# Optimization experiments

Measured on AMD Instinct MI355X. Metric: run time of the kernel, lower is better.

The kernel has to match this reference:

```python
import jax, jax.numpy as jnp
import numpy as np

B, S, N, DEG, KC = 4, 12, 8192, 16, 3
SEQ = S - KC + 1  # 10
H, LAYER, HID, MLP_H = 4, 3, 3, 64
NEG = -1e9


def setup_inputs() -> dict:
    key = jax.random.key(0)
    ks = jax.random.split(key, 40)
    f = lambda i, shp, sc=0.2: jax.random.normal(ks[i], shp, jnp.float32) * sc
    # deterministic unique edge list: DEG distinct neighbors per source node
    src = np.repeat(np.arange(N), DEG)
    dst = (src + 1 + np.tile(np.arange(DEG), N) * 37) % N
    edges = jnp.asarray(np.stack([src, dst]).astype(np.int32))
    return dict(
        occ=jax.random.normal(ks[0], (B, S, N), jnp.float32),
        prc_l=jax.random.uniform(ks[1], (B, N), jnp.float32),
        edges=edges,
        values=jnp.ones((N * DEG,), jnp.float32),
        conv_w=f(2, (1, 1, KC, 2)), conv_b=f(3, (1,)),
        gat_W=f(4, (H, SEQ, SEQ)), gat_a=f(5, (H, 2 * SEQ)),
        gat_lin_w=f(6, (1, H)), gat_lin_b=f(7, (1,)),
        gcn_w=f(8, (SEQ, SEQ)), gcn_b=f(9, (SEQ,)),
        Wih0=f(10, (4 * HID, LAYER)), Whh0=f(11, (4 * HID, HID)), bih0=f(12, (4 * HID,)), bhh0=f(13, (4 * HID,)),
        Wih1=f(14, (4 * HID, HID)), Whh1=f(15, (4 * HID, HID)), bih1=f(16, (4 * HID,)), bhh1=f(17, (4 * HID,)),
        Qw=f(18, (SEQ, SEQ)), Kw=f(19, (SEQ, SEQ)), Vw=f(20, (SEQ, SEQ)),
        m1w1=f(21, (MLP_H, SEQ)), m1b1=f(22, (MLP_H,)),
        m1w2=f(23, (MLP_H // 2, MLP_H)), m1b2=f(24, (MLP_H // 2,)),
        m1w3=f(25, (1, MLP_H // 2)), m1b3=f(26, (1,)),
        m2w1=f(27, (8 * (LAYER + 1), LAYER + 1)), m2b1=f(28, (8 * (LAYER + 1),)),
        m2w2=f(29, (4 * (LAYER + 1), 8 * (LAYER + 1))), m2b2=f(30, (4 * (LAYER + 1),)),
        m2w3=f(31, (1, 4 * (LAYER + 1))), m2b3=f(32, (1,)),
    )


def _lstm_layer(x, Wih, Whh, bih, bhh):
    # x: [T, Bn, in] time-major; PyTorch gate order i,f,g,o
    Bn, hdim = x.shape[1], Whh.shape[1]
    def step(carry, xt):
        h, c = carry
        g = xt @ Wih.T + h @ Whh.T + bih + bhh
        i, fg, gg, o = jnp.split(g, 4, axis=1)
        c = jax.nn.sigmoid(fg) * c + jax.nn.sigmoid(i) * jnp.tanh(gg)
        h = jax.nn.sigmoid(o) * jnp.tanh(c)
        return (h, c), h
    init = (jnp.zeros((Bn, hdim), x.dtype), jnp.zeros((Bn, hdim), x.dtype))
    _, hs = jax.lax.scan(step, init, x)
    return hs  # [T, Bn, hdim]


def _gat(x2, src, dst, values, mask, gat_W, gat_a, lin_w, lin_b):
    # x2: [b*n, seq]; only first N rows are gathered (faithful to the original)
    h = jnp.einsum('ns,hso->hno', x2, gat_W)                 # [H, b*n, seq]
    eh = jnp.concatenate([h[:, src, :], h[:, dst, :]], 2)    # [H, E, 2*seq]
    atts = jax.nn.leaky_relu(jnp.einsum('hed,hd->he', eh, gat_a), 0.2)  # [H, E]
    mt = atts.T @ lin_w.T + lin_b                            # [E, 1]
    new_vals = values * mt[:, 0]
    n = mask.shape[0]
    dense = jnp.zeros((n, n), x2.dtype).at[src, dst].add(new_vals)
    return jax.nn.softmax(dense + mask, axis=0)              # softmax over dim 0, as nn.Softmax(dim=0)


def reference(occ, prc_l, edges, values, conv_w, conv_b, gat_W, gat_a, gat_lin_w, gat_lin_b, gcn_w, gcn_b, Wih0, Whh0, bih0, bhh0, Wih1, Whh1, bih1, bhh1, Qw, Kw, Vw, m1w1, m1b1, m1w2, m1b2, m1w3, m1b3, m2w1, m2b1, m2w2, m2b2, m2w3, m2b3):
    b, s, n = occ.shape
    seq = s - conv_w.shape[2] + 1
    occ_t = jnp.transpose(occ, (0, 2, 1))                    # [b, n, s]
    prc = jnp.broadcast_to(prc_l[:, :, None], (b, n, s))
    fea = jnp.stack([occ_t, prc], axis=3).reshape(b * n, s, 2)[:, None]  # [bn,1,s,2]
    fea = jax.lax.conv_general_dilated(fea, conv_w, (1, 1), 'VALID',
                                       dimension_numbers=('NCHW', 'OIHW', 'NCHW'))
    fea = (fea + conv_b[None, :, None, None]).reshape(b, n, seq)
    src, dst = edges[0], edges[1]
    mask = jnp.full((n, n), NEG, occ.dtype).at[src, dst].set(0.0)
    lrelu = lambda z: jax.nn.leaky_relu(z, 0.01)
    gcn = lambda z: lrelu(z @ gcn_w.T + gcn_b)
    A1 = _gat(fea.reshape(b * n, seq), src, dst, values, mask, gat_W, gat_a, gat_lin_w, gat_lin_b)
    c1 = gcn(jnp.einsum('nm,bms->bns', A1, fea))
    A2 = _gat(c1.reshape(b * n, seq), src, dst, values, mask, gat_W, gat_a, gat_lin_w, gat_lin_b)
    c2 = gcn(jnp.einsum('nm,bms->bns', A2, c1))
    xt = jnp.stack([fea, c1, c2], axis=3).reshape(b * n, seq, 3)
    xT = jnp.transpose(xt, (1, 0, 2))                        # time-major [seq, bn, 3]
    h0 = _lstm_layer(xT, Wih0, Whh0, bih0, bhh0)
    h1 = _lstm_layer(h0, Wih1, Whh1, bih1, bhh1)
    x_long = jnp.transpose(h1, (1, 0, 2))                    # [bn, seq, 3]
    y_long = x_long[:, -1, 0]                                # [bn]
    xl = jnp.transpose(x_long, (0, 2, 1))                    # [bn, 3, seq]
    Q = xl @ Qw.T
    K = xl @ Kw.T
    V = xl @ Vw.T
    alpha = jax.nn.softmax(jnp.einsum('bis,bjs->bij', Q, K) / jnp.float32(V.shape[1]), axis=2)
    att = jnp.einsum('bij,bjs->bis', alpha, V)               # [bn, 3, seq]
    h = jax.nn.relu(att @ m1w1.T + m1b1)
    h = jax.nn.relu(h @ m1w2.T + m1b2)
    att_out = (h @ m1w3.T + m1b3)[:, :, 0]                   # [bn, 3]
    temp = jnp.concatenate([y_long[:, None], att_out], axis=1)  # [bn, 4]
    h = jax.nn.relu(temp @ m2w1.T + m2b1)
    h = jax.nn.relu(h @ m2w2.T + m2b2)
    y = (h @ m2w3.T + m2b3)[:, 0]
    return y.reshape(b, n)
```

## Files before the change

### kernel.cpp

```cpp
#include <hip/hip_runtime.h>

#define NN    8192
#define BB    4
#define SS    12
#define SEQL  10
#define SEQP  16
#define KCC   3
#define DEGN  16
#define EE    (NN*DEGN)
#define HHH   4
#define HIDN  3
#define BN    (BB*NN)

__device__ __forceinline__ float fexp(float x)  { return __expf(x); }
__device__ __forceinline__ float fsig(float x)  { return __fdividef(1.0f, 1.0f + __expf(-x)); }

__global__ __launch_bounds__(256) void k_fea_node(const float* __restrict__ occ,
                                                  const float* __restrict__ prc,
                                                  const float* __restrict__ convw,
                                                  const float* __restrict__ convb,
                                                  const float* __restrict__ gatW,
                                                  const float* __restrict__ gata,
                                                  float* __restrict__ fea,
                                                  float* __restrict__ p1p2) {
    int t = blockIdx.x * blockDim.x + threadIdx.x;
    if (t >= BN) return;
    int b = t >> 13, nn = t & (NN - 1);
    float o[SS];
    const float* op = occ + (size_t)b * SS * NN + nn;
#pragma unroll
    for (int s = 0; s < SS; s++) o[s] = op[(size_t)s * NN];
    float w0[KCC], w1s = 0.f;
#pragma unroll
    for (int k = 0; k < KCC; k++) { w0[k] = convw[k * 2]; w1s += convw[k * 2 + 1]; }
    float base = prc[t] * w1s + convb[0];
    float fv[SEQL];
#pragma unroll
    for (int tt = 0; tt < SEQL; tt++) {
        float acc = base;
#pragma unroll
        for (int k = 0; k < KCC; k++) acc += o[tt + k] * w0[k];
        fv[tt] = acc;
    }
    float* f = fea + (size_t)t * SEQP;
    *(float4*)(f)     = make_float4(fv[0], fv[1], fv[2], fv[3]);
    *(float4*)(f + 4) = make_float4(fv[4], fv[5], fv[6], fv[7]);
    *(float2*)(f + 8) = make_float2(fv[8], fv[9]);
    if (t < NN) {
#pragma unroll
        for (int hh = 0; hh < HHH; hh++) {
            float p1 = 0.f, p2 = 0.f;
#pragma unroll
            for (int oo = 0; oo < SEQL; oo++) {
                float hv = 0.f;
#pragma unroll
                for (int s = 0; s < SEQL; s++) hv += fv[s] * gatW[hh * (SEQL * SEQL) + s * SEQL + oo];
                p1 += hv * gata[hh * (2 * SEQL) + oo];
                p2 += hv * gata[hh * (2 * SEQL) + SEQL + oo];
            }
            p1p2[t * 8 + hh]     = p1;
            p1p2[t * 8 + 4 + hh] = p2;
        }
    }
}

__global__ __launch_bounds__(256) void k_colmt(const float* __restrict__ values,
                                               const float* __restrict__ p1p2,
                                               const float* __restrict__ linw,
                                               const float* __restrict__ linb,
                                               float* __restrict__ mt,
                                               float2* __restrict__ colms) {
    int u = blockIdx.x * blockDim.x + threadIdx.x;
    int q = u & 3, j = u >> 2;
    float p2l[HHH], lw[HHH];
#pragma unroll
    for (int hh = 0; hh < HHH; hh++) { p2l[hh] = p1p2[j * 8 + 4 + hh]; lw[hh] = linw[hh]; }
    float lb = linb[0];
    float v[4];
#pragma unroll
    for (int dd = 0; dd < 4; dd++) {
        int d = q * 4 + dd;
        int s = (j - 1 - d * 37) & (NN - 1);
        int e = s * DEGN + d;
        float4 p1v = *(const float4*)(p1p2 + s * 8);
        float a0 = p1v.x + p2l[0]; a0 = a0 > 0.f ? a0 : 0.2f * a0;
        float a1 = p1v.y + p2l[1]; a1 = a1 > 0.f ? a1 : 0.2f * a1;
        float a2 = p1v.z + p2l[2]; a2 = a2 > 0.f ? a2 : 0.2f * a2;
        float a3 = p1v.w + p2l[3]; a3 = a3 > 0.f ? a3 : 0.2f * a3;
        float acc = lb + a0*lw[0] + a1*lw[1] + a2*lw[2] + a3*lw[3];
        float m_ = acc * values[e];
        v[dd] = m_;
        mt[e] = m_;
    }
    float m = fmaxf(fmaxf(v[0], v[1]), fmaxf(v[2], v[3]));
    m = fmaxf(m, __shfl_xor(m, 1));
    m = fmaxf(m, __shfl_xor(m, 2));
    float sum = 0.f;
#pragma unroll
    for (int dd = 0; dd < 4; dd++) sum += fexp(v[dd] - m);
    sum += __shfl_xor(sum, 1);
    sum += __shfl_xor(sum, 2);
    if (q == 0) colms[j] = make_float2(m, __fdividef(1.0f, sum));
}

template <int DOP>
__global__ __launch_bounds__(256) void k_agg(const int* __restrict__ edges,
                                             const float* __restrict__ mt,
                                             const float2* __restrict__ colms,
                                             const float* __restrict__ xin,
                                             const float* __restrict__ gcnw,
                                             const float* __restrict__ gcnb,
                                             const float* __restrict__ gatW,
                                             const float* __restrict__ gata,
                                             float* __restrict__ xout,
                                             float* __restrict__ p1p2) {
    int u = blockIdx.x * blockDim.x + threadIdx.x;
    int q = u & 3, t = u >> 2;
    int b = t >> 13, i = t & (NN - 1);
    int e0 = i * DEGN + q * 4;
    int4   dn4 = *(const int4*)(edges + EE + e0);
    float4 mt4 = *(const float4*)(mt + e0);
    int dns[4] = {dn4.x, dn4.y, dn4.z, dn4.w};
    float mts[4] = {mt4.x, mt4.y, mt4.z, mt4.w};
    float acc[SEQL];
#pragma unroll
    for (int s = 0; s < SEQL; s++) acc[s] = 0.f;
#pragma unroll
    for (int dd = 0; dd < 4; dd++) {
        int dn = dns[dd];
        float2 ms = colms[dn];
        float w = fexp(mts[dd] - ms.x) * ms.y;
        const float* xr = xin + ((size_t)b * NN + dn) * SEQP;
        float4 v0 = *(const float4*)(xr);
        float4 v1 = *(const float4*)(xr + 4);
        float2 v2 = *(const float2*)(xr + 8);
        acc[0] += w*v0.x; acc[1] += w*v0.y; acc[2] += w*v0.z; acc[3] += w*v0.w;
        acc[4] += w*v1.x; acc[5] += w*v1.y; acc[6] += w*v1.z; acc[7] += w*v1.w;
        acc[8] += w*v2.x; acc[9] += w*v2.y;
    }
#pragma unroll
    for (int s = 0; s < SEQL; s++) acc[s] += __shfl_xor(acc[s], 1);
#pragma unroll
    for (int s = 0; s < SEQL; s++) acc[s] += __shfl_xor(acc[s], 2);

    float co[SEQL];
#pragma unroll
    for (int o = 0; o < SEQL; o++) {
        float a = gcnb[o];
#pragma unroll
        for (int s = 0; s < SEQL; s++) a += acc[s] * gcnw[o * SEQL + s];
        co[o] = a > 0.f ? a : 0.01f * a;
    }
    if (q == 0) {
        float* xo = xout + (size_t)t * SEQP;
        *(float4*)(xo)     = make_float4(co[0], co[1], co[2], co[3]);
        *(float4*)(xo + 4) = make_float4(co[4], co[5], co[6], co[7]);
        *(float2*)(xo + 8) = make_float2(co[8], co[9]);
    }
    if (DOP && t < NN) {
        float hv[SEQL];
#pragma unroll
        for (int oo = 0; oo < SEQL; oo++) hv[oo] = 0.f;
#pragma unroll
        for (int s = 0; s < SEQL; s++) {
            const float2* wr = (const float2*)(gatW + q * (SEQL*SEQL) + s * SEQL);
#pragma unroll
            for (int p = 0; p < 5; p++) {
                float2 wv = wr[p];
                hv[2*p]   += co[s] * wv.x;
                hv[2*p+1] += co[s] * wv.y;
            }
        }
        const float2* ga1 = (const float2*)(gata + q * (2*SEQL));
        const float2* ga2 = (const float2*)(gata + q * (2*SEQL) + SEQL);
        float p1 = 0.f, p2 = 0.f;
#pragma unroll
        for (int p = 0; p < 5; p++) {
            float2 a1 = ga1[p], a2 = ga2[p];
            p1 += hv[2*p] * a1.x + hv[2*p+1] * a1.y;
            p2 += hv[2*p] * a2.x + hv[2*p+1] * a2.y;
        }
        p1p2[t * 8 + q]     = p1;
        p1p2[t * 8 + 4 + q] = p2;
    }
}

__global__ __launch_bounds__(256) void k_lstm_att(
    const float* __restrict__ fea, const float* __restrict__ c1g, const float* __restrict__ c2g,
    const float* __restrict__ Wih0, const float* __restrict__ Whh0,
    const float* __restrict__ bih0, const float* __restrict__ bhh0,
    const float* __restrict__ Wih1, const float* __restrict__ Whh1,
    const float* __restrict__ bih1, const float* __restrict__ bhh1,
    const float* __restrict__ Qw, const float* __restrict__ Kw, const float* __restrict__ Vw,
    float* __restrict__ attrow) {

    int u = blockIdx.x * blockDim.x + threadIdx.x;
    int e = u & 3;
    int t = u >> 2;

    float fr[SEQL], c1r[SEQL], c2r[SEQL];
    {
        const float* a = fea + (size_t)t * SEQP;
        const float* b = c1g + (size_t)t * SEQP;
        const float* c = c2g + (size_t)t * SEQP;
        float4 a0 = *(const float4*)a, a1 = *(const float4*)(a+4); float2 a2 = *(const float2*)(a+8);
        float4 b0 = *(const float4*)b, b1 = *(const float4*)(b+4); float2 b2 = *(const float2*)(b+8);
        float4 d0 = *(const float4*)c, d1 = *(const float4*)(c+4); float2 d2 = *(const float2*)(c+8);
        fr[0]=a0.x; fr[1]=a0.y; fr[2]=a0.z; fr[3]=a0.w; fr[4]=a1.x; fr[5]=a1.y; fr[6]=a1.z; fr[7]=a1.w; fr[8]=a2.x; fr[9]=a2.y;
        c1r[0]=b0.x; c1r[1]=b0.y; c1r[2]=b0.z; c1r[3]=b0.w; c1r[4]=b1.x; c1r[5]=b1.y; c1r[6]=b1.z; c1r[7]=b1.w; c1r[8]=b2.x; c1r[9]=b2.y;
        c2r[0]=d0.x; c2r[1]=d0.y; c2r[2]=d0.z; c2r[3]=d0.w; c2r[4]=d1.x; c2r[5]=d1.y; c2r[6]=d1.z; c2r[7]=d1.w; c2r[8]=d2.x; c2r[9]=d2.y;
    }

    float W0[3][6], B0[3], W1[3][6], B1[3];
#pragma unroll
    for (int k = 0; k < 3; k++) {
        int r = e * 3 + k;
        W0[k][0]=Wih0[r*3]; W0[k][1]=Wih0[r*3+1]; W0[k][2]=Wih0[r*3+2];
        W0[k][3]=Whh0[r*3]; W0[k][4]=Whh0[r*3+1]; W0[k][5]=Whh0[r*3+2];
        B0[k]=bih0[r]+bhh0[r];
        W1[k][0]=Wih1[r*3]; W1[k][1]=Wih1[r*3+1]; W1[k][2]=Wih1[r*3+2];
        W1[k][3]=Whh1[r*3]; W1[k][4]=Whh1[r*3+1]; W1[k][5]=Whh1[r*3+2];
        B1[k]=bih1[r]+bhh1[r];
    }
    float two_e = (e == 2) ? 2.f : 1.f;
    float neg_e = (e == 2) ? -1.f : 0.f;

    float c0[3]={0,0,0}, c1s[3]={0,0,0}, h0[3]={0,0,0}, h1[3]={0,0,0};
    float hist[SEQL][HIDN];
#pragma unroll
    for (int st = 0; st < SEQL; st++) {
        float tt[3], pp[3], qq[3], rr[3];
        {
            float x0 = fr[st], x1 = c1r[st], x2 = c2r[st];
#pragma unroll
            for (int k = 0; k < 3; k++) {
                float g = B0[k] + x0*W0[k][0] + x1*W0[k][1] + x2*W0[k][2]
                                + h0[0]*W0[k][3] + h0[1]*W0[k][4] + h0[2]*W0[k][5];
                float uu = fsig(two_e * g);
                tt[k] = two_e * uu + neg_e;
            }
#pragma unroll
            for (int k = 0; k < 3; k++) pp[k] = __shfl_xor(tt[k], 1);
#pragma unroll
            for (int k = 0; k < 3; k++) { qq[k] = __shfl_xor(tt[k], 2); rr[k] = __shfl_xor(pp[k], 2); }
#pragma unroll
            for (int j = 0; j < 3; j++) {
                float si = (e==0)?tt[j]:(e==1)?pp[j]:(e==2)?qq[j]:rr[j];
                float sf = (e==0)?pp[j]:(e==1)?tt[j]:(e==2)?rr[j]:qq[j];
                float tg = (e==0)?qq[j]:(e==1)?rr[j]:(e==2)?tt[j]:pp[j];
                float so = (e==0)?rr[j]:(e==1)?qq[j]:(e==2)?pp[j]:tt[j];
                float cn = sf * c0[j] + si * tg;
                c0[j] = cn;
                h0[j] = so * (2.f * fsig(2.f * cn) - 1.f);
            }
        }
        {
#pragma unroll
            for (int k = 0; k < 3; k++) {
                float g = B1[k] + h0[0]*W1[k][0] + h0[1]*W1[k][1] + h0[2]*W1[k][2]
                                + h1[0]*W1[k][3] + h1[1]*W1[k][4] + h1[2]*W1[k][5];
                float uu = fsig(two_e * g);
                tt[k] = two_e * uu + neg_e;
            }
#pragma unroll
            for (int k = 0; k < 3; k++) pp[k] = __shfl_xor(tt[k], 1);
#pragma unroll
            for (int k = 0; k < 3; k++) { qq[k] = __shfl_xor(tt[k], 2); rr[k] = __shfl_xor(pp[k], 2); }
#pragma unroll
            for (int j = 0; j < 3; j++) {
                float si = (e==0)?tt[j]:(e==1)?pp[j]:(e==2)?qq[j]:rr[j];
                float sf = (e==0)?pp[j]:(e==1)?tt[j]:(e==2)?rr[j]:qq[j];
                float tg = (e==0)?qq[j]:(e==1)?rr[j]:(e==2)?tt[j]:pp[j];
                float so = (e==0)?rr[j]:(e==1)?qq[j]:(e==2)?pp[j]:tt[j];
                float cn = sf * c1s[j] + si * tg;
                c1s[j] = cn;
                h1[j] = so * (2.f * fsig(2.f * cn) - 1.f);
            }
        }
#pragma unroll
        for (int j = 0; j < 3; j++) hist[st][j] = h1[j];
    }

    float V[3][3];
    float sc[3][3];
#pragma unroll
    for (int a = 0; a < 3; a++)
#pragma unroll
        for (int j = 0; j < 3; j++) sc[a][j] = 0.f;
#pragma unroll
    for (int p = 0; p < 3; p++) {
        int o = 4 * p + e;
        bool act = (o < SEQL);
        int oc = act ? o : 0;
        float wq[SEQL], wk[SEQL], wv[SEQL];
        const float2* q2 = (const float2*)(Qw + oc * SEQL);
        const float2* k2 = (const float2*)(Kw + oc * SEQL);
        const float2* v2 = (const float2*)(Vw + oc * SEQL);
#pragma unroll
        for (int z = 0; z < 5; z++) {
            float2 a = q2[z], b = k2[z], c = v2[z];
            wq[2*z] = a.x; wq[2*z+1] = a.y;
            wk[2*z] = b.x; wk[2*z+1] = b.y;
            wv[2*z] = c.x; wv[2*z+1] = c.y;
        }
        float qj[3], kj[3];
#pragma unroll
        for (int j = 0; j < 3; j++) {
            float qv = 0.f, kv = 0.f, vv = 0.f;
#pragma unroll
            for (int s = 0; s < SEQL; s++) {
                float xv = hist[s][j];
                qv += xv * wq[s]; kv += xv * wk[s]; vv += xv * wv[s];
            }
            qj[j] = qv; kj[j] = kv; V[j][p] = vv;
        }
        if (act) {
#pragma unroll
            for (int a = 0; a < 3; a++)
#pragma unroll
                for (int j = 0; j < 3; j++) sc[a][j] += qj[a] * kj[j];
        }
    }
#pragma unroll
    for (int a = 0; a < 3; a++)
#pragma unroll
        for (int j = 0; j < 3; j++) {
            sc[a][j] += __shfl_xor(sc[a][j], 1);
            sc[a][j] += __shfl_xor(sc[a][j], 2);
        }

    float* ar = attrow + (size_t)t * 32;
#pragma unroll
    for (int a = 0; a < 3; a++) {
        float s0 = sc[a][0] * (1.f/3.f), s1 = sc[a][1] * (1.f/3.f), s2 = sc[a][2] * (1.f/3.f);
        float m = fmaxf(s0, fmaxf(s1, s2));
        float e0 = fexp(s0-m), e1 = fexp(s1-m), e2 = fexp(s2-m);
        float inv = __fdividef(1.0f, e0 + e1 + e2);
#pragma unroll
        for (int p = 0; p < 3; p++) {
            int o = 4 * p + e;
            if (o < SEQL)
                ar[a * SEQL + o] = (e0*V[0][p] + e1*V[1][p] + e2*V[2][p]) * inv;
        }
    }
    if (e == 0) ar[30] = hist[SEQL-1][0];
}

__global__ __launch_bounds__(256, 4) void k_head(
    const float* __restrict__ attrow,
    const float* __restrict__ m1w1, const float* __restrict__ m1b1,
    const float* __restrict__ m1w2, const float* __restrict__ m1b2,
    const float* __restrict__ m1w3, const float* __restrict__ m1b3,
    const float* __restrict__ m2w1, const float* __restrict__ m2b1,
    const float* __restrict__ m2w2, const float* __restrict__ m2b2,
    const float* __restrict__ m2w3, const float* __restrict__ m2b3,
    float* __restrict__ out) {

    __shared__ float lw[3717];
    int tid = threadIdx.x;
    for (int z = tid; z < 1024; z += 256) {
        int qq = z >> 8, kk = (z >> 4) & 15, s = z & 15;
        if (s < 12) lw[qq*200 + kk*12 + s] = (s < 10) ? m1w1[(qq*16+kk)*10 + s] : 0.f;
    }
    for (int z = tid; z < 2048; z += 256) {
        int qq = z >> 9, rem = z & 511, r = rem >> 4, kk = rem & 15;
        lw[800 + qq*520 + r*16 + kk] = m1w2[r*64 + qq*16 + kk];
    }
    for (int z = tid; z < 64;  z += 256) lw[2880 + z] = m1b1[z];
    for (int z = tid; z < 32;  z += 256) { lw[2944 + z] = m1b2[z]; lw[2976 + z] = m1w3[z]; }
    for (int z = tid; z < 128; z += 256) lw[3012 + z] = m2w1[z];
    for (int z = tid; z < 32;  z += 256) lw[3140 + z] = m2b1[z];
    for (int z = tid; z < 512; z += 256) lw[3172 + z] = m2w2[z];
    for (int z = tid; z < 16;  z += 256) { lw[3684 + z] = m2b2[z]; lw[3700 + z] = m2w3[z]; }
    if (tid == 0) { lw[3008] = m1b3[0]; lw[3716] = m2b3[0]; }
    __syncthreads();

    int u = blockIdx.x * blockDim.x + tid;
    int q = u & 3;
    int t = u >> 2;

    const float* w1b = lw + q * 200;
    float hb0[16], hb1[16], hb2a[16];
    float ylong;
    {
        float row[32];
        const float4* arp = (const float4*)(attrow + (size_t)t * 32);
#pragma unroll
        for (int p = 0; p < 8; p++) {
            float4 z = arp[p];
            row[4*p] = z.x; row[4*p+1] = z.y; row[4*p+2] = z.z; row[4*p+3] = z.w;
        }
        ylong = row[30];
#pragma unroll 4
        for (int kk = 0; kk < 16; kk++) {
            float4 wa = *(const float4*)(w1b + kk*12);
            float4 wb = *(const float4*)(w1b + kk*12 + 4);
            float4 wc = *(const float4*)(w1b + kk*12 + 8);
            float bk = lw[2880 + q*16 + kk];
            float a0 = bk
                + row[0]*wa.x + row[1]*wa.y + row[2]*wa.z + row[3]*wa.w
                + row[4]*wb.x + row[5]*wb.y + row[6]*wb.z + row[7]*wb.w
                + row[8]*wc.x + row[9]*wc.y;
            float a1 = bk
                + row[10]*wa.x + row[11]*wa.y + row[12]*wa.z + row[13]*wa.w
                + row[14]*wb.x + row[15]*wb.y + row[16]*wb.z + row[17]*wb.w
                + row[18]*wc.x + row[19]*wc.y;
            float a2 = bk
                + row[20]*wa.x + row[21]*wa.y + row[22]*wa.z + row[23]*wa.w
                + row[24]*wb.x + row[25]*wb.y + row[26]*wb.z + row[27]*wb.w
                + row[28]*wc.x + row[29]*wc.y;
            hb0[kk] = a0 > 0.f ? a0 : 0.f;
            hb1[kk] = a1 > 0.f ? a1 : 0.f;
            hb2a[kk] = a2 > 0.f ? a2 : 0.f;
        }
    }

    const float* w2b = lw + 800 + q * 520;
    float ao0 = lw[3008], ao1 = ao0, ao2 = ao0;
#pragma unroll 2
    for (int r = 0; r < 32; r++) {
        const float4* wr = (const float4*)(w2b + r * 16);
        float4 w0 = wr[0], w1 = wr[1], w2 = wr[2], w3 = wr[3];
        float p0 = hb0[0]*w0.x + hb0[1]*w0.y + hb0[2]*w0.z + hb0[3]*w0.w
                 + hb0[4]*w1.x + hb0[5]*w1.y + hb0[6]*w1.z + hb0[7]*w1.w
                 + hb0[8]*w2.x + hb0[9]*w2.y + hb0[10]*w2.z + hb0[11]*w2.w
                 + hb0[12]*w3.x + hb0[13]*w3.y + hb0[14]*w3.z + hb0[15]*w3.w;
        float p1 = hb1[0]*w0.x + hb1[1]*w0.y + hb1[2]*w0.z + hb1[3]*w0.w
                 + hb1[4]*w1.x + hb1[5]*w1.y + hb1[6]*w1.z + hb1[7]*w1.w
                 + hb1[8]*w2.x + hb1[9]*w2.y + hb1[10]*w2.z + hb1[11]*w2.w
                 + hb1[12]*w3.x + hb1[13]*w3.y + hb1[14]*w3.z + hb1[15]*w3.w;
        float p2 = hb2a[0]*w0.x + hb2a[1]*w0.y + hb2a[2]*w0.z + hb2a[3]*w0.w
                 + hb2a[4]*w1.x + hb2a[5]*w1.y + hb2a[6]*w1.z + hb2a[7]*w1.w
                 + hb2a[8]*w2.x + hb2a[9]*w2.y + hb2a[10]*w2.z + hb2a[11]*w2.w
                 + hb2a[12]*w3.x + hb2a[13]*w3.y + hb2a[14]*w3.z + hb2a[15]*w3.w;
        p0 += __shfl_xor(p0, 1); p0 += __shfl_xor(p0, 2);
        p1 += __shfl_xor(p1, 1); p1 += __shfl_xor(p1, 2);
        p2 += __shfl_xor(p2, 1); p2 += __shfl_xor(p2, 2);
        float bb = lw[2944 + r], ww = lw[2976 + r];
        float t0 = p0 + bb; t0 = t0 > 0.f ? t0 : 0.f;
        float t1 = p1 + bb; t1 = t1 > 0.f ? t1 : 0.f;
        float t2 = p2 + bb; t2 = t2 > 0.f ? t2 : 0.f;
        ao0 += t0 * ww; ao1 += t1 * ww; ao2 += t2 * ww;
    }

    float hb2[32];
#pragma unroll 8
    for (int k = 0; k < 32; k++) {
        float4 wv = *(const float4*)(lw + 3012 + k*4);
        float a = lw[3140 + k] + ylong*wv.x + ao0*wv.y + ao1*wv.z + ao2*wv.w;
        hb2[k] = a > 0.f ? a : 0.f;
    }
    float y = lw[3716];
#pragma unroll 4
    for (int r = 0; r < 16; r++) {
        float a = lw[3684 + r];
        const float4* wr = (const float4*)(lw + 3172 + r*32);
#pragma unroll
        for (int c = 0; c < 8; c++) {
            float4 wv = wr[c];
            a += hb2[4*c]*wv.x + hb2[4*c+1]*wv.y + hb2[4*c+2]*wv.z + hb2[4*c+3]*wv.w;
        }
        float h = a > 0.f ? a : 0.f;
        y += h * lw[3700 + r];
    }
    if (q == 0) out[t] = y;
}

extern "C" void kernel_launch(void* const* d_in, const int* in_sizes, int n_in,
                              void* d_out, int out_size, void* d_ws, size_t ws_size,
                              hipStream_t stream) {
    const float* occ    = (const float*)d_in[0];
    const float* prc    = (const float*)d_in[1];
    const int*   edges  = (const int*)  d_in[2];
    const float* values = (const float*)d_in[3];
    const float* convw  = (const float*)d_in[4];
    const float* convb  = (const float*)d_in[5];
    const float* gatW   = (const float*)d_in[6];
    const float* gata   = (const float*)d_in[7];
    const float* linw   = (const float*)d_in[8];
    const float* linb   = (const float*)d_in[9];
    const float* gcnw   = (const float*)d_in[10];
    const float* gcnb   = (const float*)d_in[11];
    const float* Wih0   = (const float*)d_in[12];
    const float* Whh0   = (const float*)d_in[13];
    const float* bih0   = (const float*)d_in[14];
    const float* bhh0   = (const float*)d_in[15];
    const float* Wih1   = (const float*)d_in[16];
    const float* Whh1   = (const float*)d_in[17];
    const float* bih1   = (const float*)d_in[18];
    const float* bhh1   = (const float*)d_in[19];
    const float* Qw     = (const float*)d_in[20];
    const float* Kw     = (const float*)d_in[21];
    const float* Vw     = (const float*)d_in[22];
    const float* m1w1   = (const float*)d_in[23];
    const float* m1b1   = (const float*)d_in[24];
    const float* m1w2   = (const float*)d_in[25];
    const float* m1b2   = (const float*)d_in[26];
    const float* m1w3   = (const float*)d_in[27];
    const float* m1b3   = (const float*)d_in[28];
    const float* m2w1   = (const float*)d_in[29];
    const float* m2b1   = (const float*)d_in[30];
    const float* m2w2   = (const float*)d_in[31];
    const float* m2b2   = (const float*)d_in[32];
    const float* m2w3   = (const float*)d_in[33];
    const float* m2b3   = (const float*)d_in[34];
    float* out = (float*)d_out;

    char* ws = (char*)d_ws;
    float*  fea    = (float*) (ws);
    float*  c1     = (float*) (ws + 2097152);
    float*  c2     = (float*) (ws + 4194304);
    float*  p1p2   = (float*) (ws + 6291456);
    float*  mt     = (float*) (ws + 6553600);
    float2* colms  = (float2*)(ws + 7077888);
    float*  attrow = (float*) (ws + 7143424);

    k_fea_node<<<128, 256, 0, stream>>>(occ, prc, convw, convb, gatW, gata, fea, p1p2);

    k_colmt<<<128, 256, 0, stream>>>(values, p1p2, linw, linb, mt, colms);
    k_agg<1><<<512, 256, 0, stream>>>(edges, mt, colms, fea, gcnw, gcnb,
                                      gatW, gata, c1, p1p2);

    k_colmt<<<128, 256, 0, stream>>>(values, p1p2, linw, linb, mt, colms);
    k_agg<0><<<512, 256, 0, stream>>>(edges, mt, colms, c1, gcnw, gcnb,
                                      gatW, gata, c2, p1p2);

    k_lstm_att<<<512, 256, 0, stream>>>(fea, c1, c2,
        Wih0, Whh0, bih0, bhh0, Wih1, Whh1, bih1, bhh1, Qw, Kw, Vw, attrow);

    k_head<<<512, 256, 0, stream>>>(attrow,
        m1w1, m1b1, m1w2, m1b2, m1w3, m1b3,
        m2w1, m2b1, m2w2, m2b2, m2w3, m2b3, out);
}
```

Measured before the change: 82.94 us.

## Fuse LSTM-attention and MLP head kernels; use 8 lanes per node in aggregation

Merges the LSTM/attention kernel with the MLP head kernel, so the per-node attention row stays in registers and is redistributed across the 4-lane group with shuffles instead of being written to and re-read from global memory. The head weights are staged into shared memory at the start of the fused kernel. The aggregation kernel now uses 8 lanes per node, each handling 2 edges, with one extra shuffle reduction stage, doubling the grid to expose more parallelism for the gathers. The fused kernel uses more registers (launch bounds lowered to 2 blocks per SIMD), which may reduce occupancy.

```diff
diff --git a/kernel.cpp b/kernel.cpp
--- a/kernel.cpp
+++ b/kernel.cpp
@@ -115,18 +115,18 @@
                                              float* __restrict__ xout,
                                              float* __restrict__ p1p2) {
     int u = blockIdx.x * blockDim.x + threadIdx.x;
-    int q = u & 3, t = u >> 2;
+    int q = u & 7, t = u >> 3;
     int b = t >> 13, i = t & (NN - 1);
-    int e0 = i * DEGN + q * 4;
-    int4   dn4 = *(const int4*)(edges + EE + e0);
-    float4 mt4 = *(const float4*)(mt + e0);
-    int dns[4] = {dn4.x, dn4.y, dn4.z, dn4.w};
-    float mts[4] = {mt4.x, mt4.y, mt4.z, mt4.w};
+    int e0 = i * DEGN + q * 2;
+    int2   dn2 = *(const int2*)(edges + EE + e0);
+    float2 mt2 = *(const float2*)(mt + e0);
+    int dns[2] = {dn2.x, dn2.y};
+    float mts[2] = {mt2.x, mt2.y};
     float acc[SEQL];
 #pragma unroll
     for (int s = 0; s < SEQL; s++) acc[s] = 0.f;
 #pragma unroll
-    for (int dd = 0; dd < 4; dd++) {
+    for (int dd = 0; dd < 2; dd++) {
         int dn = dns[dd];
         float2 ms = colms[dn];
         float w = fexp(mts[dd] - ms.x) * ms.y;
@@ -142,6 +142,8 @@
     for (int s = 0; s < SEQL; s++) acc[s] += __shfl_xor(acc[s], 1);
 #pragma unroll
     for (int s = 0; s < SEQL; s++) acc[s] += __shfl_xor(acc[s], 2);
+#pragma unroll
+    for (int s = 0; s < SEQL; s++) acc[s] += __shfl_xor(acc[s], 4);
 
     float co[SEQL];
 #pragma unroll
@@ -157,7 +159,7 @@
         *(float4*)(xo + 4) = make_float4(co[4], co[5], co[6], co[7]);
         *(float2*)(xo + 8) = make_float2(co[8], co[9]);
     }
-    if (DOP && t < NN) {
+    if (DOP && t < NN && q < 4) {
         float hv[SEQL];
 #pragma unroll
         for (int oo = 0; oo < SEQL; oo++) hv[oo] = 0.f;
@@ -185,16 +187,41 @@
     }
 }
 
-__global__ __launch_bounds__(256) void k_lstm_att(
+__global__ __launch_bounds__(256, 2) void k_lstm_head(
     const float* __restrict__ fea, const float* __restrict__ c1g, const float* __restrict__ c2g,
     const float* __restrict__ Wih0, const float* __restrict__ Whh0,
     const float* __restrict__ bih0, const float* __restrict__ bhh0,
     const float* __restrict__ Wih1, const float* __restrict__ Whh1,
     const float* __restrict__ bih1, const float* __restrict__ bhh1,
     const float* __restrict__ Qw, const float* __restrict__ Kw, const float* __restrict__ Vw,
-    float* __restrict__ attrow) {
-
-    int u = blockIdx.x * blockDim.x + threadIdx.x;
+    const float* __restrict__ m1w1, const float* __restrict__ m1b1,
+    const float* __restrict__ m1w2, const float* __restrict__ m1b2,
+    const float* __restrict__ m1w3, const float* __restrict__ m1b3,
+    const float* __restrict__ m2w1, const float* __restrict__ m2b1,
+    const float* __restrict__ m2w2, const float* __restrict__ m2b2,
+    const float* __restrict__ m2w3, const float* __restrict__ m2b3,
+    float* __restrict__ out) {
+
+    __shared__ float lw[3717];
+    int tid = threadIdx.x;
+    for (int z = tid; z < 1024; z += 256) {
+        int qq = z >> 8, kk = (z >> 4) & 15, s = z & 15;
+        if (s < 12) lw[qq*200 + kk*12 + s] = (s < 10) ? m1w1[(qq*16+kk)*10 + s] : 0.f;
+    }
+    for (int z = tid; z < 2048; z += 256) {
+        int qq = z >> 9, rem = z & 511, r = rem >> 4, kk = rem & 15;
+        lw[800 + qq*520 + r*16 + kk] = m1w2[r*64 + qq*16 + kk];
+    }
+    for (int z = tid; z < 64;  z += 256) lw[2880 + z] = m1b1[z];
+    for (int z = tid; z < 32;  z += 256) { lw[2944 + z] = m1b2[z]; lw[2976 + z] = m1w3[z]; }
+    for (int z = tid; z < 128; z += 256) lw[3012 + z] = m2w1[z];
+    for (int z = tid; z < 32;  z += 256) lw[3140 + z] = m2b1[z];
+    for (int z = tid; z < 512; z += 256) lw[3172 + z] = m2w2[z];
+    for (int z = tid; z < 16;  z += 256) { lw[3684 + z] = m2b2[z]; lw[3700 + z] = m2w3[z]; }
+    if (tid == 0) { lw[3008] = m1b3[0]; lw[3716] = m2b3[0]; }
+    __syncthreads();
+
+    int u = blockIdx.x * blockDim.x + tid;
     int e = u & 3;
     int t = u >> 2;
 
@@ -229,7 +256,7 @@
     float hist[SEQL][HIDN];
 #pragma unroll
     for (int st = 0; st < SEQL; st++) {
-        float tt[3], pp[3], qq[3], rr[3];
+        float tt[3], pp[3], qq2[3], rr[3];
         {
             float x0 = fr[st], x1 = c1r[st], x2 = c2r[st];
 #pragma unroll
@@ -242,13 +269,13 @@
 #pragma unroll
             for (int k = 0; k < 3; k++) pp[k] = __shfl_xor(tt[k], 1);
 #pragma unroll
-            for (int k = 0; k < 3; k++) { qq[k] = __shfl_xor(tt[k], 2); rr[k] = __shfl_xor(pp[k], 2); }
+            for (int k = 0; k < 3; k++) { qq2[k] = __shfl_xor(tt[k], 2); rr[k] = __shfl_xor(pp[k], 2); }
 #pragma unroll
             for (int j = 0; j < 3; j++) {
-                float si = (e==0)?tt[j]:(e==1)?pp[j]:(e==2)?qq[j]:rr[j];
-                float sf = (e==0)?pp[j]:(e==1)?tt[j]:(e==2)?rr[j]:qq[j];
-                float tg = (e==0)?qq[j]:(e==1)?rr[j]:(e==2)?tt[j]:pp[j];
-                float so = (e==0)?rr[j]:(e==1)?qq[j]:(e==2)?pp[j]:tt[j];
+                float si = (e==0)?tt[j]:(e==1)?pp[j]:(e==2)?qq2[j]:rr[j];
+                float sf = (e==0)?pp[j]:(e==1)?tt[j]:(e==2)?rr[j]:qq2[j];
+                float tg = (e==0)?qq2[j]:(e==1)?rr[j]:(e==2)?tt[j]:pp[j];
+                float so = (e==0)?rr[j]:(e==1)?qq2[j]:(e==2)?pp[j]:tt[j];
                 float cn = sf * c0[j] + si * tg;
                 c0[j] = cn;
                 h0[j] = so * (2.f * fsig(2.f * cn) - 1.f);
@@ -265,13 +292,13 @@
 #pragma unroll
             for (int k = 0; k < 3; k++) pp[k] = __shfl_xor(tt[k], 1);
 #pragma unroll
-            for (int k = 0; k < 3; k++) { qq[k] = __shfl_xor(tt[k], 2); rr[k] = __shfl_xor(pp[k], 2); }
+            for (int k = 0; k < 3; k++) { qq2[k] = __shfl_xor(tt[k], 2); rr[k] = __shfl_xor(pp[k], 2); }
 #pragma unroll
             for (int j = 0; j < 3; j++) {
-                float si = (e==0)?tt[j]:(e==1)?pp[j]:(e==2)?qq[j]:rr[j];
-                float sf = (e==0)?pp[j]:(e==1)?tt[j]:(e==2)?rr[j]:qq[j];
-                float tg = (e==0)?qq[j]:(e==1)?rr[j]:(e==2)?tt[j]:pp[j];
-                float so = (e==0)?rr[j]:(e==1)?qq[j]:(e==2)?pp[j]:tt[j];
+                float si = (e==0)?tt[j]:(e==1)?pp[j]:(e==2)?qq2[j]:rr[j];
+                float sf = (e==0)?pp[j]:(e==1)?tt[j]:(e==2)?rr[j]:qq2[j];
+                float tg = (e==0)?qq2[j]:(e==1)?rr[j]:(e==2)?tt[j]:pp[j];
+                float so = (e==0)?rr[j]:(e==1)?qq2[j]:(e==2)?pp[j]:tt[j];
                 float cn = sf * c1s[j] + si * tg;
                 c1s[j] = cn;
                 h1[j] = so * (2.f * fsig(2.f * cn) - 1.f);
@@ -329,7 +356,7 @@
             sc[a][j] += __shfl_xor(sc[a][j], 2);
         }
 
-    float* ar = attrow + (size_t)t * 32;
+    float row[32];
 #pragma unroll
     for (int a = 0; a < 3; a++) {
         float s0 = sc[a][0] * (1.f/3.f), s1 = sc[a][1] * (1.f/3.f), s2 = sc[a][2] * (1.f/3.f);
@@ -338,86 +365,52 @@
         float inv = __fdividef(1.0f, e0 + e1 + e2);
 #pragma unroll
         for (int p = 0; p < 3; p++) {
-            int o = 4 * p + e;
-            if (o < SEQL)
-                ar[a * SEQL + o] = (e0*V[0][p] + e1*V[1][p] + e2*V[2][p]) * inv;
-        }
-    }
-    if (e == 0) ar[30] = hist[SEQL-1][0];
-}
-
-__global__ __launch_bounds__(256, 4) void k_head(
-    const float* __restrict__ attrow,
-    const float* __restrict__ m1w1, const float* __restrict__ m1b1,
-    const float* __restrict__ m1w2, const float* __restrict__ m1b2,
-    const float* __restrict__ m1w3, const float* __restrict__ m1b3,
-    const float* __restrict__ m2w1, const float* __restrict__ m2b1,
-    const float* __restrict__ m2w2, const float* __restrict__ m2b2,
-    const float* __restrict__ m2w3, const float* __restrict__ m2b3,
-    float* __restrict__ out) {
-
-    __shared__ float lw[3717];
-    int tid = threadIdx.x;
-    for (int z = tid; z < 1024; z += 256) {
-        int qq = z >> 8, kk = (z >> 4) & 15, s = z & 15;
-        if (s < 12) lw[qq*200 + kk*12 + s] = (s < 10) ? m1w1[(qq*16+kk)*10 + s] : 0.f;
-    }
-    for (int z = tid; z < 2048; z += 256) {
-        int qq = z >> 9, rem = z & 511, r = rem >> 4, kk = rem & 15;
-        lw[800 + qq*520 + r*16 + kk] = m1w2[r*64 + qq*16 + kk];
-    }
-    for (int z = tid; z < 64;  z += 256) lw[2880 + z] = m1b1[z];
-    for (int z = tid; z < 32;  z += 256) { lw[2944 + z] = m1b2[z]; lw[2976 + z] = m1w3[z]; }
-    for (int z = tid; z < 128; z += 256) lw[3012 + z] = m2w1[z];
-    for (int z = tid; z < 32;  z += 256) lw[3140 + z] = m2b1[z];
-    for (int z = tid; z < 512; z += 256) lw[3172 + z] = m2w2[z];
-    for (int z = tid; z < 16;  z += 256) { lw[3684 + z] = m2b2[z]; lw[3700 + z] = m2w3[z]; }
-    if (tid == 0) { lw[3008] = m1b3[0]; lw[3716] = m2b3[0]; }
-    __syncthreads();
-
-    int u = blockIdx.x * blockDim.x + tid;
-    int q = u & 3;
-    int t = u >> 2;
-
+            float av  = (e0*V[0][p] + e1*V[1][p] + e2*V[2][p]) * inv;
+            float av1 = __shfl_xor(av, 1);
+            float av2 = __shfl_xor(av, 2);
+            float av3 = __shfl_xor(av1, 2);
+#pragma unroll
+            for (int c = 0; c < 4; c++) {
+                int o = 4 * p + c;
+                if (o < SEQL)
+                    row[a * SEQL + o] = (e == c) ? av
+                                      : ((e ^ 1) == c) ? av1
+                                      : ((e ^ 2) == c) ? av2 : av3;
+            }
+        }
+    }
+    float ylong = hist[SEQL-1][0];
+    row[30] = ylong; row[31] = 0.f;
+
+    int q = e;
     const float* w1b = lw + q * 200;
     float hb0[16], hb1[16], hb2a[16];
-    float ylong;
-    {
-        float row[32];
-        const float4* arp = (const float4*)(attrow + (size_t)t * 32);
-#pragma unroll
-        for (int p = 0; p < 8; p++) {
-            float4 z = arp[p];
-            row[4*p] = z.x; row[4*p+1] = z.y; row[4*p+2] = z.z; row[4*p+3] = z.w;
-        }
-        ylong = row[30];
 #pragma unroll 4
-        for (int kk = 0; kk < 16; kk++) {
-            float4 wa = *(const float4*)(w1b + kk*12);
-            float4 wb = *(const float4*)(w1b + kk*12 + 4);
-            float4 wc = *(const float4*)(w1b + kk*12 + 8);
-            float bk = lw[2880 + q*16 + kk];
-            float a0 = bk
-                + row[0]*wa.x + row[1]*wa.y + row[2]*wa.z + row[3]*wa.w
-                + row[4]*wb.x + row[5]*wb.y + row[6]*wb.z + row[7]*wb.w
-                + row[8]*wc.x + row[9]*wc.y;
-            float a1 = bk
-                + row[10]*wa.x + row[11]*wa.y + row[12]*wa.z + row[13]*wa.w
-                + row[14]*wb.x + row[15]*wb.y + row[16]*wb.z + row[17]*wb.w
-                + row[18]*wc.x + row[19]*wc.y;
-            float a2 = bk
-                + row[20]*wa.x + row[21]*wa.y + row[22]*wa.z + row[23]*wa.w
-                + row[24]*wb.x + row[25]*wb.y + row[26]*wb.z + row[27]*wb.w
-                + row[28]*wc.x + row[29]*wc.y;
-            hb0[kk] = a0 > 0.f ? a0 : 0.f;
-            hb1[kk] = a1 > 0.f ? a1 : 0.f;
-            hb2a[kk] = a2 > 0.f ? a2 : 0.f;
-        }
+    for (int kk = 0; kk < 16; kk++) {
+        float4 wa = *(const float4*)(w1b + kk*12);
+        float4 wb = *(const float4*)(w1b + kk*12 + 4);
+        float4 wc = *(const float4*)(w1b + kk*12 + 8);
+        float bk = lw[2880 + q*16 + kk];
+        float a0 = bk
+            + row[0]*wa.x + row[1]*wa.y + row[2]*wa.z + row[3]*wa.w
+            + row[4]*wb.x + row[5]*wb.y + row[6]*wb.z + row[7]*wb.w
+            + row[8]*wc.x + row[9]*wc.y;
+        float a1 = bk
+            + row[10]*wa.x + row[11]*wa.y + row[12]*wa.z + row[13]*wa.w
+            + row[14]*wb.x + row[15]*wb.y + row[16]*wb.z + row[17]*wb.w
+            + row[18]*wc.x + row[19]*wc.y;
+        float a2 = bk
+            + row[20]*wa.x + row[21]*wa.y + row[22]*wa.z + row[23]*wa.w
+            + row[24]*wb.x + row[25]*wb.y + row[26]*wb.z + row[27]*wb.w
+            + row[28]*wc.x + row[29]*wc.y;
+        hb0[kk] = a0 > 0.f ? a0 : 0.f;
+        hb1[kk] = a1 > 0.f ? a1 : 0.f;
+        hb2a[kk] = a2 > 0.f ? a2 : 0.f;
     }
 
     const float* w2b = lw + 800 + q * 520;
     float ao0 = lw[3008], ao1 = ao0, ao2 = ao0;
-#pragma unroll 2
+#pragma unroll 4
     for (int r = 0; r < 32; r++) {
         const float4* wr = (const float4*)(w2b + r * 16);
         float4 w0 = wr[0], w1 = wr[1], w2 = wr[2], w3 = wr[3];
@@ -513,22 +506,19 @@
     float*  p1p2   = (float*) (ws + 6291456);
     float*  mt     = (float*) (ws + 6553600);
     float2* colms  = (float2*)(ws + 7077888);
-    float*  attrow = (float*) (ws + 7143424);
 
     k_fea_node<<<128, 256, 0, stream>>>(occ, prc, convw, convb, gatW, gata, fea, p1p2);
 
     k_colmt<<<128, 256, 0, stream>>>(values, p1p2, linw, linb, mt, colms);
-    k_agg<1><<<512, 256, 0, stream>>>(edges, mt, colms, fea, gcnw, gcnb,
-                                      gatW, gata, c1, p1p2);
+    k_agg<1><<<1024, 256, 0, stream>>>(edges, mt, colms, fea, gcnw, gcnb,
+                                       gatW, gata, c1, p1p2);
 
     k_colmt<<<128, 256, 0, stream>>>(values, p1p2, linw, linb, mt, colms);
-    k_agg<0><<<512, 256, 0, stream>>>(edges, mt, colms, c1, gcnw, gcnb,
-                                      gatW, gata, c2, p1p2);
-
-    k_lstm_att<<<512, 256, 0, stream>>>(fea, c1, c2,
-        Wih0, Whh0, bih0, bhh0, Wih1, Whh1, bih1, bhh1, Qw, Kw, Vw, attrow);
-
-    k_head<<<512, 256, 0, stream>>>(attrow,
+    k_agg<0><<<1024, 256, 0, stream>>>(edges, mt, colms, c1, gcnw, gcnb,
+                                       gatW, gata, c2, p1p2);
+
+    k_lstm_head<<<512, 256, 0, stream>>>(fea, c1, c2,
+        Wih0, Whh0, bih0, bhh0, Wih1, Whh1, bih1, bhh1, Qw, Kw, Vw,
         m1w1, m1b1, m1w2, m1b2, m1w3, m1b3,
         m2w1, m2b1, m2w2, m2b2, m2w3, m2b3, out);
 }
```

Result: faster. 76.62 us (-7.6%).
